# Optimization experiments

Hardware: AMD Instinct MI355X
Metric: run time of the kernel (lower is better)

The kernel has to match this reference:

```python
import jax, jax.numpy as jnp
import numpy as np

VOCAB_SIZE = 16384
BETA = 0.25
RESI_RATIO = 0.5  # abs(quant_resi=-0.5); kernel size 3


def setup_inputs() -> dict:
    key = jax.random.key(0)
    k1, k2, k3 = jax.random.split(key, 3)
    B, C, h, w = 16, 32, 32, 32
    f_BChw = jax.random.normal(k1, (B, C, h, w), dtype=jnp.float32)
    emb_weight = jax.random.normal(k2, (VOCAB_SIZE, C), dtype=jnp.float32)
    conv_w = jax.random.normal(k3, (C, C, 3, 3), dtype=jnp.float32) * 0.05
    conv_b = jnp.zeros((C,), dtype=jnp.float32)
    return {"f_BChw": f_BChw, "emb_weight": emb_weight, "conv_w": conv_w, "conv_b": conv_b}


def _res_conv(h_BChw, conv_w, conv_b):
    # ResConv: h*(1-r) + conv3x3(h)*r
    y = jax.lax.conv_general_dilated(
        h_BChw, conv_w, window_strides=(1, 1), padding=((1, 1), (1, 1)),
        dimension_numbers=("NCHW", "OIHW", "NCHW"))
    y = y + conv_b[None, :, None, None]
    return h_BChw * (1.0 - RESI_RATIO) + y * RESI_RATIO


def reference(f_BChw, emb_weight, conv_w, conv_b):
    f_BChw = f_BChw.astype(jnp.float32)
    B, C, h, w = f_BChw.shape
    query_NxC = jax.lax.stop_gradient(f_BChw).transpose(0, 2, 3, 1).reshape(-1, C)  # [N,C]
    # vocab_norm=False path: squared Euclidean distance via ||q||^2 + ||e||^2 - 2 q e^T
    E_dist = (jnp.sum(query_NxC * query_NxC, axis=1, keepdims=True)
              + jnp.sum(emb_weight * emb_weight, axis=1)
              - 2.0 * (query_NxC @ emb_weight.T))  # [N, vocab]
    idx_N = jnp.argmin(E_dist, axis=1)  # [N]
    # bincount for usage stats
    counts = jnp.zeros((VOCAB_SIZE,), dtype=jnp.float32).at[idx_N].add(1.0)
    # embedding gather -> [B,h,w,C] -> [B,C,h,w]
    zq_BChw = emb_weight[idx_N].reshape(B, h, w, C).transpose(0, 3, 1, 2)
    fhat_BChw = _res_conv(zq_BChw, conv_w, conv_b)
    vq_loss = (BETA * jnp.mean((jax.lax.stop_gradient(fhat_BChw) - f_BChw) ** 2)
               + jnp.mean((fhat_BChw - jax.lax.stop_gradient(f_BChw)) ** 2))
    # straight-through estimator
    fhat_out = f_BChw + jax.lax.stop_gradient(fhat_BChw - f_BChw)
    prob = counts / jnp.sum(counts)
    vocab_usage = jnp.mean((prob > 0.01 / VOCAB_SIZE).astype(jnp.float32)) * 100.0
    return fhat_out, vq_loss, vocab_usage
```

## Files before the change

kernel.cpp:

```cpp
#include <hip/hip_runtime.h>

#define VOCAB 16384
#define N_Q   16384
#define C     32
#define HW    1024
#define VCH   16
#define CODES_PER_CH 1024
#define TILES_PER_CH 64
#define CHUNKB 147456

typedef _Float16 half8 __attribute__((ext_vector_type(8)));
typedef float f32x4  __attribute__((ext_vector_type(4)));

__global__ __launch_bounds__(256) void k_prepE(const float* __restrict__ emb,
                                               char* __restrict__ Eblob,
                                               const float* __restrict__ convw,
                                               float* __restrict__ wp,
                                               unsigned long long* __restrict__ keys,
                                               int* __restrict__ counts,
                                               int* __restrict__ done) {
    int bx = blockIdx.x;
    if (bx >= 64) {
        if (bx == 64) {
            for (int k = threadIdx.x; k < C * C * 9; k += 256) {
                int cout = k / (C * 9);
                int r = k % (C * 9);
                int cin = r / 9;
                int tap = r % 9;
                wp[(tap * C + cin) * C + cout] = convw[k];
            }
        } else if (bx == 65) {
            for (int k = threadIdx.x; k < VOCAB; k += 256) keys[k] = ~0ULL;
        } else {
            for (int k = threadIdx.x; k < VOCAB; k += 256) counts[k] = 0;
            if (threadIdx.x == 0) *done = 0;
        }
        return;
    }
    int j = bx * 256 + threadIdx.x;
    const float4* e4 = reinterpret_cast<const float4*>(emb + j * C);
    float s = 0.f;
    float v[C];
#pragma unroll
    for (int k = 0; k < 8; ++k) {
        float4 t = e4[k];
        v[4 * k] = t.x; v[4 * k + 1] = t.y; v[4 * k + 2] = t.z; v[4 * k + 3] = t.w;
        s += t.x * t.x + t.y * t.y + t.z * t.z + t.w * t.w;
    }
    float en2 = 0.5f * s;
    int chunkid = j >> 10;
    int t = (j >> 4) & 63;
    char* gb = Eblob + (size_t)chunkid * CHUNKB;
    *reinterpret_cast<float4*>(gb + 131072 + t * 256 + (j & 15) * 16)
        = make_float4(en2, en2, en2, en2);
#pragma unroll
    for (int ko = 0; ko < 4; ++ko) {
        half8 vh, vl;
#pragma unroll
        for (int e = 0; e < 8; ++e) {
            float x = v[ko * 8 + e];
            _Float16 h = (_Float16)x;
            vh[e] = h;
            vl[e] = (_Float16)(x - (float)h);
        }
        int lane = (ko << 4) | (j & 15);
        *reinterpret_cast<half8*>(gb + t * 1024 + lane * 16) = vh;
        *reinterpret_cast<half8*>(gb + 65536 + t * 1024 + lane * 16) = vl;
    }
}

__global__ __launch_bounds__(256, 4) void k_argmin(
    const float* __restrict__ f,
    const char* __restrict__ Eblob,
    unsigned long long* __restrict__ keys) {
    int tid = threadIdx.x;
    int lane = tid & 63;
    int w = tid >> 6;
    int wid = blockIdx.x * 4 + w;
    int chunk = blockIdx.y;

    half8 a_hi[4], a_lo[4];
    int c0 = (lane >> 4) * 8;
#pragma unroll
    for (int qq = 0; qq < 4; ++qq) {
        int n = (wid * 4 + qq) * 16 + (lane & 15);
        int b = n >> 10, rem = n & 1023;
        const float* fp = f + (b * C + c0) * HW + rem;
#pragma unroll
        for (int e = 0; e < 8; ++e) {
            float x = -fp[e * HW];
            _Float16 h = (_Float16)x;
            a_hi[qq][e] = h;
            a_lo[qq][e] = (_Float16)(x - (float)h);
        }
    }

    float best[4][4];
#pragma unroll
    for (int qq = 0; qq < 4; ++qq)
#pragma unroll
        for (int r = 0; r < 4; ++r) best[qq][r] = __uint_as_float(0x7F800000u);

    unsigned mpack = 0xFFFFFFC0u;
    asm("" : "+v"(mpack));

    const char* gb  = Eblob + (size_t)chunk * CHUNKB;
    const char* gbl = gb + lane * 16;
    const char* gel = gb + 131072 + (lane & 15) * 16;

    for (int tt = 0; tt < TILES_PER_CH; ++tt) {
        half8 bh = *(const half8*)(gbl + tt * 1024);
        half8 bl = *(const half8*)(gbl + 65536 + tt * 1024);
        f32x4 eq = *(const f32x4*)(gel + tt * 256);
        unsigned t = (unsigned)tt;
#pragma unroll
        for (int qq = 0; qq < 4; ++qq) {
            f32x4 acc = __builtin_amdgcn_mfma_f32_16x16x32_f16(a_hi[qq], bh, eq, 0, 0, 0);
            acc = __builtin_amdgcn_mfma_f32_16x16x32_f16(a_hi[qq], bl, acc, 0, 0, 0);
            acc = __builtin_amdgcn_mfma_f32_16x16x32_f16(a_lo[qq], bh, acc, 0, 0, 0);
#pragma unroll
            for (int r = 0; r < 4; ++r) {
                unsigned p = (__float_as_uint(acc[r]) & mpack) | t;
                best[qq][r] = fminf(best[qq][r], __uint_as_float(p));
            }
        }
    }

#pragma unroll
    for (int qq = 0; qq < 4; ++qq)
#pragma unroll
        for (int r = 0; r < 4; ++r) {
            float d = best[qq][r];
            int t = (int)(__float_as_uint(d) & 63u);
            int code = chunk * CODES_PER_CH + (t << 4) + (lane & 15);
#pragma unroll
            for (int m = 1; m < 16; m <<= 1) {
                float od = __shfl_xor(d, m, 64);
                int oc = __shfl_xor(code, m, 64);
                if (od < d || (od == d && oc < code)) { d = od; code = oc; }
            }
            if ((lane & 15) == 0) {
                int row = ((lane >> 4) * 4) + r;
                int n = (wid * 4 + qq) * 16 + row;
                unsigned bits = __float_as_uint(d);
                unsigned s = ((int)bits >= 0) ? (bits | 0x80000000u) : ~bits;
                unsigned long long key = ((unsigned long long)s << 32) | (unsigned)code;
                atomicMin(&keys[n], key);
            }
        }
}

__global__ __launch_bounds__(256) void k_conv(const unsigned long long* __restrict__ keys,
                                              const float* __restrict__ emb,
                                              const float* __restrict__ wp,
                                              const float* __restrict__ bias,
                                              const float* __restrict__ f,
                                              int* __restrict__ counts,
                                              float* __restrict__ out,
                                              float* __restrict__ lpart,
                                              int* __restrict__ done) {
    __shared__ float sZ[128 * 33];
    __shared__ float sW[9216];
    __shared__ float red[256];
    __shared__ int sfin;
    int blk = blockIdx.x;
    int b = blk >> 4;
    int r0 = (blk & 15) * 2;
    int tid = threadIdx.x;

    {
        float4* dW = reinterpret_cast<float4*>(sW);
        const float4* sWp = reinterpret_cast<const float4*>(wp);
        for (int i = tid; i < 2304; i += 256) dW[i] = sWp[i];
    }
    {
        int px = tid >> 1, half = tid & 1;
        int row = px >> 5, col = px & 31;
        int gy = r0 - 1 + row;
        float* d = &sZ[px * 33 + half * 16];
        if (gy >= 0 && gy < 32) {
            int id = (int)(keys[b * HW + gy * 32 + col] & 0xFFFFFFFFULL);
            const float4* s = reinterpret_cast<const float4*>(emb + id * C + half * 16);
#pragma unroll
            for (int k = 0; k < 4; ++k) {
                float4 v = s[k];
                d[4 * k] = v.x; d[4 * k + 1] = v.y; d[4 * k + 2] = v.z; d[4 * k + 3] = v.w;
            }
        } else {
#pragma unroll
            for (int k = 0; k < 16; ++k) d[k] = 0.f;
        }
    }
    __syncthreads();

    int tx = tid & 31, ty = (tid >> 5) & 1, cg = tid >> 6;
    int co0 = cg * 8;
    int gy = r0 + ty;
    if (cg == 0) {
        int id = (int)(keys[b * HW + gy * 32 + tx] & 0xFFFFFFFFULL);
        atomicAdd(&counts[id], 1);
    }
    float acc[8];
#pragma unroll
    for (int u = 0; u < 8; ++u) acc[u] = bias[co0 + u];
    for (int dy = -1; dy <= 1; ++dy) {
        for (int dx = -1; dx <= 1; ++dx) {
            int gx = tx + dx;
            if (gx < 0 || gx >= 32) continue;
            const float* zp = &sZ[((ty + 1 + dy) * 32 + gx) * 33];
            int tap = (dy + 1) * 3 + (dx + 1);
            const float* wtap = &sW[tap * C * C + co0];
#pragma unroll
            for (int cin = 0; cin < C; ++cin) {
                float z = zp[cin];
                const f32x4* w4 = reinterpret_cast<const f32x4*>(wtap + cin * C);
                f32x4 wa = w4[0], wb = w4[1];
#pragma unroll
                for (int u = 0; u < 4; ++u) acc[u] = fmaf(z, wa[u], acc[u]);
#pragma unroll
                for (int u = 0; u < 4; ++u) acc[4 + u] = fmaf(z, wb[u], acc[4 + u]);
            }
        }
    }
    float lsum = 0.f;
#pragma unroll
    for (int u = 0; u < 8; ++u) {
        int cc = co0 + u;
        float zqv = sZ[((ty + 1) * 32 + tx) * 33 + cc];
        float fh = 0.5f * (zqv + acc[u]);
        int off = (b * C + cc) * HW + gy * 32 + tx;
        out[off] = fh;
        float diff = fh - f[off];
        lsum += diff * diff;
    }
    red[tid] = lsum;
    __syncthreads();
    for (int s = 128; s > 0; s >>= 1) {
        if (tid < s) red[tid] += red[tid + s];
        __syncthreads();
    }
    if (tid == 0) lpart[blk] = red[0];

    if (tid == 0) {
        __threadfence();
        int v = atomicAdd(done, 1);
        sfin = (v == 255) ? 1 : 0;
    }
    __syncthreads();
    if (sfin) {
        __threadfence();
        int* redi = (int*)sZ;
        int used = 0;
        for (int i = tid; i < VOCAB; i += 256) used += (counts[i] != 0) ? 1 : 0;
        red[tid] = lpart[tid];
        redi[tid] = used;
        __syncthreads();
        for (int s = 128; s > 0; s >>= 1) {
            if (tid < s) { red[tid] += red[tid + s]; redi[tid] += redi[tid + s]; }
            __syncthreads();
        }
        if (tid == 0) {
            out[N_Q * C]     = 1.25f * red[0] / (float)(N_Q * C);
            out[N_Q * C + 1] = 100.f * (float)redi[0] / (float)VOCAB;
        }
    }
}

extern "C" void kernel_launch(void* const* d_in, const int* in_sizes, int n_in,
                              void* d_out, int out_size, void* d_ws, size_t ws_size,
                              hipStream_t stream) {
    const float* f     = (const float*)d_in[0];
    const float* emb   = (const float*)d_in[1];
    const float* convw = (const float*)d_in[2];
    const float* convb = (const float*)d_in[3];
    float* out = (float*)d_out;
    float* ws  = (float*)d_ws;

    float*  wp     = ws;
    float*  lpart  = ws + 9216;
    int*    done   = (int*)(ws + 9472);
    int*    counts = (int*)(ws + 9488);
    unsigned long long* keys = (unsigned long long*)(ws + 25872);
    char*   Eblob  = (char*)(ws + 58640);

    k_prepE<<<67, 256, 0, stream>>>(emb, Eblob, convw, wp, keys, counts, done);
    dim3 g2(64, VCH);
    k_argmin<<<g2, 256, 0, stream>>>(f, Eblob, keys);
    k_conv<<<256, 256, 0, stream>>>(keys, emb, wp, convb, f, counts, out, lpart, done);
}
```

Measured before the change: 109.1 us.

## Double-buffer codebook tiles into LDS via async global_load_lds per wave

Replaces the direct global loads of codebook tiles in the argmin kernel with per-wave double-buffered staging into LDS using global_load_lds, prefetching the next group of four tiles while computing the current one. Occupancy hint is lowered from 4 to 2 blocks per CU to make room for the shared buffers. The aim is to hide global memory latency behind the MFMA work. In exchange it adds LDS traffic, relies on hand-placed waitcnt counts, and reduces wave-level parallelism.

```diff
diff --git a/kernel.cpp b/kernel.cpp
--- a/kernel.cpp
+++ b/kernel.cpp
@@ -8,6 +8,7 @@
 #define CODES_PER_CH 1024
 #define TILES_PER_CH 64
 #define CHUNKB 147456
+#define WBUF   9216
 
 typedef _Float16 half8 __attribute__((ext_vector_type(8)));
 typedef float f32x4  __attribute__((ext_vector_type(4)));
@@ -69,15 +70,33 @@
     }
 }
 
-__global__ __launch_bounds__(256, 4) void k_argmin(
+__device__ __forceinline__ void stage_grp(const char* gb, int g, char* db, int lane) {
+#pragma unroll
+    for (int c = 0; c < 4; ++c)
+        __builtin_amdgcn_global_load_lds(
+            (const __attribute__((address_space(1))) void*)(gb + g * 4096 + c * 1024 + lane * 16),
+            (__attribute__((address_space(3))) void*)(db + c * 1024 + lane * 16), 16, 0, 0);
+#pragma unroll
+    for (int c = 0; c < 4; ++c)
+        __builtin_amdgcn_global_load_lds(
+            (const __attribute__((address_space(1))) void*)(gb + 65536 + g * 4096 + c * 1024 + lane * 16),
+            (__attribute__((address_space(3))) void*)(db + 4096 + c * 1024 + lane * 16), 16, 0, 0);
+    __builtin_amdgcn_global_load_lds(
+        (const __attribute__((address_space(1))) void*)(gb + 131072 + g * 1024 + lane * 16),
+        (__attribute__((address_space(3))) void*)(db + 8192 + lane * 16), 16, 0, 0);
+}
+
+__global__ __launch_bounds__(256, 2) void k_argmin(
     const float* __restrict__ f,
     const char* __restrict__ Eblob,
     unsigned long long* __restrict__ keys) {
+    __shared__ __align__(16) char lds[4 * 2 * WBUF];
     int tid = threadIdx.x;
     int lane = tid & 63;
     int w = tid >> 6;
     int wid = blockIdx.x * 4 + w;
     int chunk = blockIdx.y;
+    char* buf0 = lds + w * (2 * WBUF);
 
     half8 a_hi[4], a_lo[4];
     int c0 = (lane >> 4) * 8;
@@ -104,24 +123,35 @@
     unsigned mpack = 0xFFFFFFC0u;
     asm("" : "+v"(mpack));
 
-    const char* gb  = Eblob + (size_t)chunk * CHUNKB;
-    const char* gbl = gb + lane * 16;
-    const char* gel = gb + 131072 + (lane & 15) * 16;
-
-    for (int tt = 0; tt < TILES_PER_CH; ++tt) {
-        half8 bh = *(const half8*)(gbl + tt * 1024);
-        half8 bl = *(const half8*)(gbl + 65536 + tt * 1024);
-        f32x4 eq = *(const f32x4*)(gel + tt * 256);
-        unsigned t = (unsigned)tt;
-#pragma unroll
-        for (int qq = 0; qq < 4; ++qq) {
-            f32x4 acc = __builtin_amdgcn_mfma_f32_16x16x32_f16(a_hi[qq], bh, eq, 0, 0, 0);
-            acc = __builtin_amdgcn_mfma_f32_16x16x32_f16(a_hi[qq], bl, acc, 0, 0, 0);
-            acc = __builtin_amdgcn_mfma_f32_16x16x32_f16(a_lo[qq], bh, acc, 0, 0, 0);
-#pragma unroll
-            for (int r = 0; r < 4; ++r) {
-                unsigned p = (__float_as_uint(acc[r]) & mpack) | t;
-                best[qq][r] = fminf(best[qq][r], __uint_as_float(p));
+    const char* gb = Eblob + (size_t)chunk * CHUNKB;
+
+    stage_grp(gb, 0, buf0, lane);
+
+    for (int g = 0; g < 16; ++g) {
+        if (g < 15) {
+            stage_grp(gb, g + 1, buf0 + ((g + 1) & 1) * WBUF, lane);
+            asm volatile("s_waitcnt vmcnt(9)" ::: "memory");
+        } else {
+            asm volatile("s_waitcnt vmcnt(0)" ::: "memory");
+        }
+        __builtin_amdgcn_sched_barrier(0);
+        const char* bb = buf0 + (g & 1) * WBUF;
+#pragma unroll
+        for (int tt = 0; tt < 4; ++tt) {
+            half8 bh = *(const half8*)(bb + tt * 1024 + lane * 16);
+            half8 bl = *(const half8*)(bb + 4096 + tt * 1024 + lane * 16);
+            f32x4 eq = *(const f32x4*)(bb + 8192 + tt * 256 + (lane & 15) * 16);
+            unsigned t = (unsigned)(g * 4 + tt);
+#pragma unroll
+            for (int qq = 0; qq < 4; ++qq) {
+                f32x4 acc = __builtin_amdgcn_mfma_f32_16x16x32_f16(a_hi[qq], bh, eq, 0, 0, 0);
+                acc = __builtin_amdgcn_mfma_f32_16x16x32_f16(a_hi[qq], bl, acc, 0, 0, 0);
+                acc = __builtin_amdgcn_mfma_f32_16x16x32_f16(a_lo[qq], bh, acc, 0, 0, 0);
+#pragma unroll
+                for (int r = 0; r < 4; ++r) {
+                    unsigned p = (__float_as_uint(acc[r]) & mpack) | t;
+                    best[qq][r] = fminf(best[qq][r], __uint_as_float(p));
+                }
             }
         }
     }
```

After: 97.91 us. -10.3%, faster.
